# Optimization experiments

Hardware: AMD Instinct MI355X
Metric: run time of the kernel (lower is better)

The kernel has to match this reference:

```python
import jax, jax.numpy as jnp
import numpy as np

NUM_HEADS = 8
NUM_GROUPS = 32
EPS = 1e-5


def group_norm(x, gamma, beta):
    # x: [B, C, H, W]; normalize over (C//G, H, W) within each of G groups
    B, C, H, W = x.shape
    xg = x.reshape(B, NUM_GROUPS, C // NUM_GROUPS, H, W)
    mean = xg.mean(axis=(2, 3, 4), keepdims=True)
    var = xg.var(axis=(2, 3, 4), keepdims=True)
    xn = ((xg - mean) * jax.lax.rsqrt(var + EPS)).reshape(B, C, H, W)
    return xn * gamma[None, :, None, None] + beta[None, :, None, None]


def setup_inputs() -> dict:
    key = jax.random.key(0)
    ks = jax.random.split(key, 7)
    B, C, H, W = 16, 512, 32, 32
    x = jax.random.normal(ks[0], (B, C, H, W), dtype=jnp.float32)
    gamma = jnp.ones((C,), dtype=jnp.float32)
    beta = jnp.zeros((C,), dtype=jnp.float32)
    # 1x1 convs == per-pixel linear layers
    w_qkv = jax.random.normal(ks[1], (3 * C, C), dtype=jnp.float32) * (1.0 / np.sqrt(C))
    b_qkv = jax.random.normal(ks[2], (3 * C,), dtype=jnp.float32) * 0.02
    w_proj = jax.random.normal(ks[3], (C, C), dtype=jnp.float32) * (1.0 / np.sqrt(C))
    b_proj = jax.random.normal(ks[4], (C,), dtype=jnp.float32) * 0.02
    return {"x": x, "gamma": gamma, "beta": beta, "w_qkv": w_qkv,
            "b_qkv": b_qkv, "w_proj": w_proj, "b_proj": b_proj}


def reference(x, gamma, beta, w_qkv, b_qkv, w_proj, b_proj):
    B, C, H, W = x.shape
    nh = NUM_HEADS
    d = C // nh
    N = H * W
    h = group_norm(x, gamma, beta)
    # 1x1 conv: [B,C,H,W] x [3C,C] -> [B,3C,H,W]
    qkv = jnp.einsum('bchw,oc->bohw', h, w_qkv) + b_qkv[None, :, None, None]
    qkv = qkv.reshape(B, 3, nh, d, N)  # matches torch reshape(B,3,heads,d,HW)
    q, k, v = qkv[:, 0], qkv[:, 1], qkv[:, 2]
    scale = d ** (-0.5)
    attn = jnp.einsum('bhdn,bhdm->bhnm', q, k) * scale  # [B,h,N,N]
    attn = jax.nn.softmax(attn, axis=-1)
    out = jnp.einsum('bhnm,bhdm->bhdn', attn, v)  # [B,h,d,N]
    out = out.reshape(B, C, H, W)
    proj = jnp.einsum('bchw,oc->bohw', out, w_proj) + b_proj[None, :, None, None]
    return x + proj
```

## Files before the change

### kernel.cpp

```cpp
#include <hip/hip_runtime.h>
#include <cstddef>

#define B_  16
#define C_  512
#define N_  1024

typedef __attribute__((ext_vector_type(8))) __bf16 bf16x8;
typedef __attribute__((ext_vector_type(4))) float f32x4;
typedef __attribute__((ext_vector_type(4))) short s16x4;

__device__ __forceinline__ unsigned short f2bf(float x) {
  unsigned u = __float_as_uint(x);
  return (unsigned short)((u + 0x7fffu + ((u >> 16) & 1u)) >> 16);
}
__device__ __forceinline__ float bf2f(unsigned short h) {
  return __uint_as_float(((unsigned)h) << 16);
}

#define GLDS16(g, l)                                                            \
  __builtin_amdgcn_global_load_lds(                                             \
      (const __attribute__((address_space(1))) void*)(g),                       \
      (__attribute__((address_space(3))) void*)(l), 16, 0, 0)

__global__ __launch_bounds__(256) void wconv_kernel(
    const float* __restrict__ wq, const float* __restrict__ wp,
    unsigned short* __restrict__ oq, unsigned short* __restrict__ op) {
  int i = blockIdx.x * 256 + threadIdx.x;
  const float4* src; unsigned short* dst; int off;
  if (i < 196608) { src = (const float4*)wq; dst = oq; off = i; }
  else            { src = (const float4*)wp; dst = op; off = i - 196608; }
  float4 v = src[off];
  union { unsigned short s[4]; ushort4 u; } o;
  o.s[0] = f2bf(v.x); o.s[1] = f2bf(v.y);
  o.s[2] = f2bf(v.z); o.s[3] = f2bf(v.w);
  *(ushort4*)(dst + (size_t)off * 4) = o.u;
}

__global__ __launch_bounds__(256) void gn_kernel(
    const float* __restrict__ x, const float* __restrict__ gamma,
    const float* __restrict__ beta, unsigned short* __restrict__ hT) {
  int bg = blockIdx.x;
  int b = bg >> 5, g = bg & 31;
  size_t base = ((size_t)b * C_ + (size_t)g * 16) * N_;
  const float4* x4 = (const float4*)(x + base);
  int tid = threadIdx.x;

  float sum = 0.f, sq = 0.f;
  float4 vv[16];
#pragma unroll
  for (int i = 0; i < 16; i++) {
    float4 v = x4[tid + i * 256];
    vv[i] = v;
    sum += v.x + v.y + v.z + v.w;
    sq  += v.x * v.x + v.y * v.y + v.z * v.z + v.w * v.w;
  }
#pragma unroll
  for (int off = 32; off > 0; off >>= 1) {
    sum += __shfl_down(sum, off, 64);
    sq  += __shfl_down(sq, off, 64);
  }
  __shared__ float sm[4], sv[4];
  int lane = tid & 63, w = tid >> 6;
  if (lane == 0) { sm[w] = sum; sv[w] = sq; }
  __syncthreads();
  if (tid == 0) {
    float s = sm[0] + sm[1] + sm[2] + sm[3];
    float q = sv[0] + sv[1] + sv[2] + sv[3];
    float mean = s * (1.f / 16384.f);
    float var  = q * (1.f / 16384.f) - mean * mean;
    sm[0] = mean;
    sv[0] = rsqrtf(var + 1e-5f);
  }
  __syncthreads();
  float mean = sm[0], rstd = sv[0];

  union { unsigned short s[16]; uint4 u[2]; } row[4];
#pragma unroll
  for (int i = 0; i < 16; i++) {
    int c = g * 16 + i;
    float ga = gamma[c] * rstd;
    float be = beta[c] - mean * ga;
    float4 v = vv[i];
    row[0].s[i] = f2bf(v.x * ga + be);
    row[1].s[i] = f2bf(v.y * ga + be);
    row[2].s[i] = f2bf(v.z * ga + be);
    row[3].s[i] = f2bf(v.w * ga + be);
  }
#pragma unroll
  for (int j = 0; j < 4; j++) {
    uint4* dst = (uint4*)(hT + ((size_t)b * N_ + 4 * tid + j) * C_ + g * 16);
    dst[0] = row[j].u[0];
    dst[1] = row[j].u[1];
  }
}

template <int OUT_BF16>
__global__ __launch_bounds__(256) void gemm_mfma(
    const unsigned short* __restrict__ Wb, const float* __restrict__ bias,
    const unsigned short* __restrict__ InT, const float* __restrict__ resid,
    void* __restrict__ Out, int M) {
  __shared__ __align__(16) unsigned short As[128 * 32];
  __shared__ __align__(16) unsigned short Bs[128 * 32];

  const int b = blockIdx.z;
  const int n0 = blockIdx.x * 128, m0 = blockIdx.y * 128;
  const int tid = threadIdx.x;
  const int lane = tid & 63, wave = tid >> 6;
  const int col = lane & 15, quad = lane >> 4;
  const int wm = (wave >> 1) << 6, wn = (wave & 1) << 6;

  const unsigned short* Ag = Wb + (size_t)m0 * C_;
  const unsigned short* Bg = InT + ((size_t)b * N_ + n0) * C_;

  const int r0 = tid >> 2, c0 = (tid & 3) << 3;

  f32x4 acc[4][4];
#pragma unroll
  for (int i = 0; i < 4; i++)
#pragma unroll
    for (int j = 0; j < 4; j++) acc[i][j] = f32x4{0.f, 0.f, 0.f, 0.f};

  for (int k0 = 0; k0 < C_; k0 += 32) {
    __syncthreads();
    GLDS16(Ag + (size_t)r0 * C_ + k0 + c0,        &As[tid * 8]);
    GLDS16(Ag + (size_t)(r0 + 64) * C_ + k0 + c0, &As[(tid + 256) * 8]);
    GLDS16(Bg + (size_t)r0 * C_ + k0 + c0,        &Bs[tid * 8]);
    GLDS16(Bg + (size_t)(r0 + 64) * C_ + k0 + c0, &Bs[(tid + 256) * 8]);
    __syncthreads();

    bf16x8 af[4], bfr[4];
#pragma unroll
    for (int mt = 0; mt < 4; mt++)
      af[mt] = *(const bf16x8*)&As[(wm + mt * 16 + col) * 32 + quad * 8];
#pragma unroll
    for (int nt = 0; nt < 4; nt++)
      bfr[nt] = *(const bf16x8*)&Bs[(wn + nt * 16 + col) * 32 + quad * 8];
#pragma unroll
    for (int mt = 0; mt < 4; mt++)
#pragma unroll
      for (int nt = 0; nt < 4; nt++)
        acc[mt][nt] = __builtin_amdgcn_mfma_f32_16x16x32_bf16(
            af[mt], bfr[nt], acc[mt][nt], 0, 0, 0);
  }

#pragma unroll
  for (int mt = 0; mt < 4; mt++) {
    int mbase = m0 + wm + mt * 16 + quad * 4;
#pragma unroll
    for (int nt = 0; nt < 4; nt++) {
      int n = n0 + wn + nt * 16 + col;
#pragma unroll
      for (int r = 0; r < 4; r++) {
        int m = mbase + r;
        float v = acc[mt][nt][r] + bias[m];
        size_t off = ((size_t)b * M + m) * N_ + n;
        if constexpr (OUT_BF16) {
          ((unsigned short*)Out)[off] = f2bf(v);
        } else {
          ((float*)Out)[off] = v + resid[off];
        }
      }
    }
  }
}

__global__ __launch_bounds__(256) void attn_mfma(
    const unsigned short* __restrict__ qkv, unsigned short* __restrict__ aoT) {
  __shared__ __align__(16) unsigned short Kt[64 * 72];
  __shared__ __align__(16) unsigned short Vs[64 * 72];

  const int tid = threadIdx.x;
  const int wave = tid >> 6, lane = tid & 63;
  const int quad = lane >> 4, col = lane & 15;
  const int b = blockIdx.z, hh = blockIdx.y;
  const int qblk = blockIdx.x * 256 + wave * 64;

  const unsigned short* qp = qkv + ((size_t)b * 1536 + hh * 64) * N_;
  const unsigned short* kp = qp + (size_t)512 * N_;
  const unsigned short* vp = qp + (size_t)1024 * N_;

  bf16x8 qf[4][2];
#pragma unroll
  for (int nt = 0; nt < 4; nt++) {
    int qg = qblk + nt * 16 + col;
#pragma unroll
    for (int ks = 0; ks < 2; ks++) {
      union { unsigned short s[8]; bf16x8 v; } t;
#pragma unroll
      for (int j = 0; j < 8; j++) {
        int d = ks * 32 + quad * 8 + j;
        t.s[j] = f2bf(0.125f * bf2f(qp[(size_t)d * N_ + qg]));
      }
      qf[nt][ks] = t.v;
    }
  }

  float l_i[4];
  f32x4 O[4][4];
#pragma unroll
  for (int nt = 0; nt < 4; nt++) {
    l_i[nt] = 0.f;
#pragma unroll
    for (int mt = 0; mt < 4; mt++) O[mt][nt] = f32x4{0.f, 0.f, 0.f, 0.f};
  }

  const int sc = tid & 15, sd0 = tid >> 4;

  for (int kt = 0; kt < 16; kt++) {
    __syncthreads();
#pragma unroll
    for (int i = 0; i < 4; i++) {
      int d = sd0 + 16 * i;
      ushort4 kv = *(const ushort4*)(kp + (size_t)d * N_ + kt * 64 + sc * 4);
      ushort4 vv = *(const ushort4*)(vp + (size_t)d * N_ + kt * 64 + sc * 4);
      int sw = (sc >> 1) & 7;
      int dcol = (((d >> 3) ^ sw) << 3) | (d & 7);
      Kt[(4 * sc + 0) * 72 + dcol] = kv.x;
      Kt[(4 * sc + 1) * 72 + dcol] = kv.y;
      Kt[(4 * sc + 2) * 72 + dcol] = kv.z;
      Kt[(4 * sc + 3) * 72 + dcol] = kv.w;
      unsigned short* vrow = &Vs[d * 72 + 4 * sc];
      vrow[0] = vv.x; vrow[1] = vv.y;
      vrow[2] = vv.z; vrow[3] = vv.w;
    }
    __syncthreads();

    bf16x8 kf[4][2];
#pragma unroll
    for (int mt = 0; mt < 4; mt++) {
      int key = 16 * mt + col;
      int swr = (key >> 3) & 7;
#pragma unroll
      for (int ks = 0; ks < 2; ks++)
        kf[mt][ks] = *(const bf16x8*)&Kt[key * 72 + (((ks * 4 + quad) ^ swr) << 3)];
    }
    s16x4 vf[4][4];
#pragma unroll
    for (int mt = 0; mt < 4; mt++)
#pragma unroll
      for (int kc = 0; kc < 4; kc++)
        vf[mt][kc] = *(const s16x4*)&Vs[(16 * mt + col) * 72 + 16 * kc + quad * 4];

#pragma unroll
    for (int nt = 0; nt < 4; nt++) {
      f32x4 sf[4];
#pragma unroll
      for (int mt = 0; mt < 4; mt++) sf[mt] = f32x4{0.f, 0.f, 0.f, 0.f};
#pragma unroll
      for (int ks = 0; ks < 2; ks++)
#pragma unroll
        for (int mt = 0; mt < 4; mt++)
          sf[mt] = __builtin_amdgcn_mfma_f32_16x16x32_bf16(kf[mt][ks], qf[nt][ks], sf[mt], 0, 0, 0);

      s16x4 pb[4];
      float lsum = 0.f;
#pragma unroll
      for (int kc = 0; kc < 4; kc++) {
        float e0 = __expf(sf[kc][0]);
        float e1 = __expf(sf[kc][1]);
        float e2 = __expf(sf[kc][2]);
        float e3 = __expf(sf[kc][3]);
        lsum += (e0 + e1) + (e2 + e3);
        unsigned lo = __builtin_amdgcn_perm(__float_as_uint(e1), __float_as_uint(e0), 0x07060302u);
        unsigned hi = __builtin_amdgcn_perm(__float_as_uint(e3), __float_as_uint(e2), 0x07060302u);
        union { unsigned u[2]; s16x4 v; } t;
        t.u[0] = lo; t.u[1] = hi;
        pb[kc] = t.v;
      }
      l_i[nt] += lsum;

#pragma unroll
      for (int kc = 0; kc < 4; kc++)
#pragma unroll
        for (int mt = 0; mt < 4; mt++)
          O[mt][nt] = __builtin_amdgcn_mfma_f32_16x16x16bf16_1k(vf[mt][kc], pb[kc], O[mt][nt], 0, 0, 0);
    }
  }

#pragma unroll
  for (int nt = 0; nt < 4; nt++) {
    float ls = l_i[nt];
    ls += __shfl_xor(ls, 16, 64);
    ls += __shfl_xor(ls, 32, 64);
    float inv = 1.f / ls;
    int qg = qblk + nt * 16 + col;
    unsigned short* dst = aoT + ((size_t)b * N_ + qg) * C_ + hh * 64;
#pragma unroll
    for (int mt = 0; mt < 4; mt++) {
      union { unsigned short s[4]; ushort4 v; } o;
#pragma unroll
      for (int r = 0; r < 4; r++) o.s[r] = f2bf(O[mt][nt][r] * inv);
      *(ushort4*)(dst + mt * 16 + quad * 4) = o.v;
    }
  }
}

extern "C" void kernel_launch(void* const* d_in, const int* in_sizes, int n_in,
                              void* d_out, int out_size, void* d_ws, size_t ws_size,
                              hipStream_t stream) {
  (void)in_sizes; (void)n_in; (void)out_size; (void)ws_size;
  const float* x      = (const float*)d_in[0];
  const float* gamma  = (const float*)d_in[1];
  const float* beta   = (const float*)d_in[2];
  const float* w_qkv  = (const float*)d_in[3];
  const float* b_qkv  = (const float*)d_in[4];
  const float* w_proj = (const float*)d_in[5];
  const float* b_proj = (const float*)d_in[6];
  float* out = (float*)d_out;

  unsigned short* hT   = (unsigned short*)d_ws;
  unsigned short* qkvb = hT + (size_t)B_ * N_ * C_;
  unsigned short* aoT  = hT;
  unsigned short* wqb  = qkvb + (size_t)B_ * 1536 * N_;
  unsigned short* wpb  = wqb + (size_t)1536 * 512;

  wconv_kernel<<<dim3(1024), dim3(256), 0, stream>>>(w_qkv, w_proj, wqb, wpb);
  gn_kernel<<<dim3(B_ * 32), dim3(256), 0, stream>>>(x, gamma, beta, hT);
  gemm_mfma<1><<<dim3(8, 12, 16), dim3(256), 0, stream>>>(
      wqb, b_qkv, hT, (const float*)nullptr, (void*)qkvb, 1536);
  attn_mfma<<<dim3(4, 8, 16), dim3(256), 0, stream>>>(qkvb, aoT);
  gemm_mfma<0><<<dim3(8, 4, 16), dim3(256), 0, stream>>>(
      wpb, b_proj, aoT, x, (void*)out, 512);
}
```

Measured before the change: 225.9 us.

## Write Q/K transposed from QKV GEMM and double-buffer V via async LDS loads

The QKV GEMM epilogue now writes Q and K in token-major layout with vectorized stores. Q is pre-scaled by the softmax scale times log2(e), so attention can use exp2 and load Q and K fragments directly from global memory. V keeps its channel-major layout and is staged into a swizzled, double-buffered LDS tile with global_load_lds, which removes the per-tile LDS transpose and one barrier. The PV product moves to the 16x16x32 MFMA by pairing key tiles. K fragments now come from global memory every tile, which may add memory traffic or latency in exchange for less LDS work.

```diff
diff --git a/kernel.cpp b/kernel.cpp
--- a/kernel.cpp
+++ b/kernel.cpp
@@ -4,17 +4,14 @@
 #define B_  16
 #define C_  512
 #define N_  1024
+#define QSC 0.18033688011112042f
 
 typedef __attribute__((ext_vector_type(8))) __bf16 bf16x8;
 typedef __attribute__((ext_vector_type(4))) float f32x4;
-typedef __attribute__((ext_vector_type(4))) short s16x4;
 
 __device__ __forceinline__ unsigned short f2bf(float x) {
   unsigned u = __float_as_uint(x);
   return (unsigned short)((u + 0x7fffu + ((u >> 16) & 1u)) >> 16);
-}
-__device__ __forceinline__ float bf2f(unsigned short h) {
-  return __uint_as_float(((unsigned)h) << 16);
 }
 
 #define GLDS16(g, l)                                                            \
@@ -94,11 +91,11 @@
   }
 }
 
-template <int OUT_BF16>
+template <int MODE>
 __global__ __launch_bounds__(256) void gemm_mfma(
     const unsigned short* __restrict__ Wb, const float* __restrict__ bias,
     const unsigned short* __restrict__ InT, const float* __restrict__ resid,
-    void* __restrict__ Out, int M) {
+    void* __restrict__ Out, void* __restrict__ Out2, int M) {
   __shared__ __align__(16) unsigned short As[128 * 32];
   __shared__ __align__(16) unsigned short Bs[128 * 32];
 
@@ -143,31 +140,60 @@
             af[mt], bfr[nt], acc[mt][nt], 0, 0, 0);
   }
 
-#pragma unroll
-  for (int mt = 0; mt < 4; mt++) {
-    int mbase = m0 + wm + mt * 16 + quad * 4;
-#pragma unroll
-    for (int nt = 0; nt < 4; nt++) {
-      int n = n0 + wn + nt * 16 + col;
-#pragma unroll
-      for (int r = 0; r < 4; r++) {
-        int m = mbase + r;
-        float v = acc[mt][nt][r] + bias[m];
-        size_t off = ((size_t)b * M + m) * N_ + n;
-        if constexpr (OUT_BF16) {
-          ((unsigned short*)Out)[off] = f2bf(v);
-        } else {
-          ((float*)Out)[off] = v + resid[off];
+  if constexpr (MODE == 0) {
+#pragma unroll
+    for (int mt = 0; mt < 4; mt++) {
+      int mbase = m0 + wm + mt * 16 + quad * 4;
+#pragma unroll
+      for (int nt = 0; nt < 4; nt++) {
+        int n = n0 + wn + nt * 16 + col;
+#pragma unroll
+        for (int r = 0; r < 4; r++) {
+          int m = mbase + r;
+          size_t off = ((size_t)b * M + m) * N_ + n;
+          ((float*)Out)[off] = acc[mt][nt][r] + bias[m] + resid[off];
         }
       }
     }
+  } else {
+    if (blockIdx.y < 8) {
+      float qs = (blockIdx.y < 4) ? QSC : 1.0f;
+#pragma unroll
+      for (int mt = 0; mt < 4; mt++) {
+        int mbase = m0 + wm + mt * 16 + quad * 4;
+#pragma unroll
+        for (int nt = 0; nt < 4; nt++) {
+          int n = n0 + wn + nt * 16 + col;
+          union { unsigned short s[4]; ushort4 v; } o;
+#pragma unroll
+          for (int r = 0; r < 4; r++)
+            o.s[r] = f2bf((acc[mt][nt][r] + bias[mbase + r]) * qs);
+          *(ushort4*)((unsigned short*)Out + ((size_t)b * N_ + n) * 1024 + mbase) = o.v;
+        }
+      }
+    } else {
+#pragma unroll
+      for (int mt = 0; mt < 4; mt++) {
+        int mbase = m0 + wm + mt * 16 + quad * 4;
+#pragma unroll
+        for (int nt = 0; nt < 4; nt++) {
+          int n = n0 + wn + nt * 16 + col;
+#pragma unroll
+          for (int r = 0; r < 4; r++) {
+            int m = mbase + r;
+            ((unsigned short*)Out2)[((size_t)b * 512 + (m - 1024)) * N_ + n] =
+                f2bf(acc[mt][nt][r] + bias[m]);
+          }
+        }
+      }
+    }
   }
 }
 
 __global__ __launch_bounds__(256) void attn_mfma(
-    const unsigned short* __restrict__ qkv, unsigned short* __restrict__ aoT) {
-  __shared__ __align__(16) unsigned short Kt[64 * 72];
-  __shared__ __align__(16) unsigned short Vs[64 * 72];
+    const unsigned short* __restrict__ qkT, const unsigned short* __restrict__ Vb,
+    unsigned short* __restrict__ aoT) {
+  __shared__ __align__(16) unsigned short Vs[2][64 * 64];
 
   const int tid = threadIdx.x;
   const int wave = tid >> 6, lane = tid & 63;
@@ -175,25 +201,19 @@
   const int b = blockIdx.z, hh = blockIdx.y;
   const int qblk = blockIdx.x * 256 + wave * 64;
 
-  const unsigned short* qp = qkv + ((size_t)b * 1536 + hh * 64) * N_;
-  const unsigned short* kp = qp + (size_t)512 * N_;
-  const unsigned short* vp = qp + (size_t)1024 * N_;
+  const unsigned short* qkrow = qkT + (size_t)b * N_ * 1024;
+  const unsigned short* vp = Vb + ((size_t)b * 512 + hh * 64) * N_;
 
   bf16x8 qf[4][2];
 #pragma unroll
   for (int nt = 0; nt < 4; nt++) {
-    int qg = qblk + nt * 16 + col;
-#pragma unroll
-    for (int ks = 0; ks < 2; ks++) {
-      union { unsigned short s[8]; bf16x8 v; } t;
-#pragma unroll
-      for (int j = 0; j < 8; j++) {
-        int d = ks * 32 + quad * 8 + j;
-        t.s[j] = f2bf(0.125f * bf2f(qp[(size_t)d * N_ + qg]));
-      }
-      qf[nt][ks] = t.v;
-    }
-  }
+    const unsigned short* qr = qkrow + (size_t)(qblk + nt * 16 + col) * 1024 + hh * 64;
+#pragma unroll
+    for (int ks = 0; ks < 2; ks++)
+      qf[nt][ks] = *(const bf16x8*)(qr + ks * 32 + quad * 8);
+  }
+
+  const int krow_base = 8 * (col >> 2) + (col & 3);
 
   float l_i[4];
   f32x4 O[4][4];
@@ -204,76 +224,72 @@
     for (int mt = 0; mt < 4; mt++) O[mt][nt] = f32x4{0.f, 0.f, 0.f, 0.f};
   }
 
-  const int sc = tid & 15, sd0 = tid >> 4;
+  const int sd = tid >> 3, ss = tid & 7;
+  const int sc0 = (ss ^ (sd & 7)) * 8;
+  const int sc1 = (ss ^ ((sd + 32) & 7)) * 8;
+
+#define STAGE_V(p, kt)                                                          \
+  do {                                                                          \
+    GLDS16(vp + (size_t)sd * N_ + (kt) * 64 + sc0, &Vs[p][tid * 8]);            \
+    GLDS16(vp + (size_t)(sd + 32) * N_ + (kt) * 64 + sc1,                       \
+           &Vs[p][(tid + 256) * 8]);                                            \
+  } while (0)
+
+  STAGE_V(0, 0);
 
   for (int kt = 0; kt < 16; kt++) {
+    const int p = kt & 1;
     __syncthreads();
-#pragma unroll
-    for (int i = 0; i < 4; i++) {
-      int d = sd0 + 16 * i;
-      ushort4 kv = *(const ushort4*)(kp + (size_t)d * N_ + kt * 64 + sc * 4);
-      ushort4 vv = *(const ushort4*)(vp + (size_t)d * N_ + kt * 64 + sc * 4);
-      int sw = (sc >> 1) & 7;
-      int dcol = (((d >> 3) ^ sw) << 3) | (d & 7);
-      Kt[(4 * sc + 0) * 72 + dcol] = kv.x;
-      Kt[(4 * sc + 1) * 72 + dcol] = kv.y;
-      Kt[(4 * sc + 2) * 72 + dcol] = kv.z;
-      Kt[(4 * sc + 3) * 72 + dcol] = kv.w;
-      unsigned short* vrow = &Vs[d * 72 + 4 * sc];
-      vrow[0] = vv.x; vrow[1] = vv.y;
-      vrow[2] = vv.z; vrow[3] = vv.w;
-    }
-    __syncthreads();
+    if (kt < 15) STAGE_V(p ^ 1, kt + 1);
 
     bf16x8 kf[4][2];
 #pragma unroll
+    for (int u = 0; u < 4; u++) {
+      int krow = kt * 64 + 32 * (u >> 1) + 4 * (u & 1) + krow_base;
+      const unsigned short* kr = qkrow + (size_t)krow * 1024 + 512 + hh * 64;
+#pragma unroll
+      for (int ks = 0; ks < 2; ks++)
+        kf[u][ks] = *(const bf16x8*)(kr + ks * 32 + quad * 8);
+    }
+
+    bf16x8 vf[4][2];
+#pragma unroll
     for (int mt = 0; mt < 4; mt++) {
-      int key = 16 * mt + col;
-      int swr = (key >> 3) & 7;
-#pragma unroll
-      for (int ks = 0; ks < 2; ks++)
-        kf[mt][ks] = *(const bf16x8*)&Kt[key * 72 + (((ks * 4 + quad) ^ swr) << 3)];
-    }
-    s16x4 vf[4][4];
-#pragma unroll
-    for (int mt = 0; mt < 4; mt++)
-#pragma unroll
-      for (int kc = 0; kc < 4; kc++)
-        vf[mt][kc] = *(const s16x4*)&Vs[(16 * mt + col) * 72 + 16 * kc + quad * 4];
+      int d = 16 * mt + col;
+#pragma unroll
+      for (int s = 0; s < 2; s++)
+        vf[mt][s] = *(const bf16x8*)&Vs[p][d * 64 + (((4 * s + quad) ^ (d & 7)) << 3)];
+    }
 
 #pragma unroll
     for (int nt = 0; nt < 4; nt++) {
-      f32x4 sf[4];
-#pragma unroll
-      for (int mt = 0; mt < 4; mt++) sf[mt] = f32x4{0.f, 0.f, 0.f, 0.f};
-#pragma unroll
-      for (int ks = 0; ks < 2; ks++)
+#pragma unroll
+      for (int s = 0; s < 2; s++) {
+        f32x4 sfA = f32x4{0.f, 0.f, 0.f, 0.f};
+        f32x4 sfB = f32x4{0.f, 0.f, 0.f, 0.f};
+#pragma unroll
+        for (int ks = 0; ks < 2; ks++) {
+          sfA = __builtin_amdgcn_mfma_f32_16x16x32_bf16(kf[2 * s][ks], qf[nt][ks], sfA, 0, 0, 0);
+          sfB = __builtin_amdgcn_mfma_f32_16x16x32_bf16(kf[2 * s + 1][ks], qf[nt][ks], sfB, 0, 0, 0);
+        }
+        float eA0 = __builtin_amdgcn_exp2f(sfA[0]);
+        float eA1 = __builtin_amdgcn_exp2f(sfA[1]);
+        float eA2 = __builtin_amdgcn_exp2f(sfA[2]);
+        float eA3 = __builtin_amdgcn_exp2f(sfA[3]);
+        float eB0 = __builtin_amdgcn_exp2f(sfB[0]);
+        float eB1 = __builtin_amdgcn_exp2f(sfB[1]);
+        float eB2 = __builtin_amdgcn_exp2f(sfB[2]);
+        float eB3 = __builtin_amdgcn_exp2f(sfB[3]);
+        l_i[nt] += ((eA0 + eA1) + (eA2 + eA3)) + ((eB0 + eB1) + (eB2 + eB3));
+        union { unsigned u[4]; bf16x8 v; } pf;
+        pf.u[0] = __builtin_amdgcn_perm(__float_as_uint(eA1), __float_as_uint(eA0), 0x07060302u);
+        pf.u[1] = __builtin_amdgcn_perm(__float_as_uint(eA3), __float_as_uint(eA2), 0x07060302u);
+        pf.u[2] = __builtin_amdgcn_perm(__float_as_uint(eB1), __float_as_uint(eB0), 0x07060302u);
+        pf.u[3] = __builtin_amdgcn_perm(__float_as_uint(eB3), __float_as_uint(eB2), 0x07060302u);
 #pragma unroll
         for (int mt = 0; mt < 4; mt++)
-          sf[mt] = __builtin_amdgcn_mfma_f32_16x16x32_bf16(kf[mt][ks], qf[nt][ks], sf[mt], 0, 0, 0);
-
-      s16x4 pb[4];
-      float lsum = 0.f;
-#pragma unroll
-      for (int kc = 0; kc < 4; kc++) {
-        float e0 = __expf(sf[kc][0]);
-        float e1 = __expf(sf[kc][1]);
-        float e2 = __expf(sf[kc][2]);
-        float e3 = __expf(sf[kc][3]);
-        lsum += (e0 + e1) + (e2 + e3);
-        unsigned lo = __builtin_amdgcn_perm(__float_as_uint(e1), __float_as_uint(e0), 0x07060302u);
-        unsigned hi = __builtin_amdgcn_perm(__float_as_uint(e3), __float_as_uint(e2), 0x07060302u);
-        union { unsigned u[2]; s16x4 v; } t;
-        t.u[0] = lo; t.u[1] = hi;
-        pb[kc] = t.v;
+          O[mt][nt] = __builtin_amdgcn_mfma_f32_16x16x32_bf16(vf[mt][s], pf.v, O[mt][nt], 0, 0, 0);
       }
-      l_i[nt] += lsum;
-
-#pragma unroll
-      for (int kc = 0; kc < 4; kc++)
-#pragma unroll
-        for (int mt = 0; mt < 4; mt++)
-          O[mt][nt] = __builtin_amdgcn_mfma_f32_16x16x16bf16_1k(vf[mt][kc], pb[kc], O[mt][nt], 0, 0, 0);
     }
   }
 
@@ -293,6 +309,7 @@
       *(ushort4*)(dst + mt * 16 + quad * 4) = o.v;
     }
   }
+#undef STAGE_V
 }
 
 extern "C" void kernel_launch(void* const* d_in, const int* in_sizes, int n_in,
@@ -308,17 +325,18 @@
   const float* b_proj = (const float*)d_in[6];
   float* out = (float*)d_out;
 
-  unsigned short* hT   = (unsigned short*)d_ws;
-  unsigned short* qkvb = hT + (size_t)B_ * N_ * C_;
-  unsigned short* aoT  = hT;
-  unsigned short* wqb  = qkvb + (size_t)B_ * 1536 * N_;
-  unsigned short* wpb  = wqb + (size_t)1536 * 512;
+  unsigned short* hT  = (unsigned short*)d_ws;
+  unsigned short* qkT = hT + (size_t)B_ * N_ * C_;
+  unsigned short* Vb  = qkT + (size_t)B_ * N_ * 1024;
+  unsigned short* aoT = hT;
+  unsigned short* wqb = Vb + (size_t)B_ * C_ * N_;
+  unsigned short* wpb = wqb + (size_t)1536 * 512;
 
   wconv_kernel<<<dim3(1024), dim3(256), 0, stream>>>(w_qkv, w_proj, wqb, wpb);
   gn_kernel<<<dim3(B_ * 32), dim3(256), 0, stream>>>(x, gamma, beta, hT);
   gemm_mfma<1><<<dim3(8, 12, 16), dim3(256), 0, stream>>>(
-      wqb, b_qkv, hT, (const float*)nullptr, (void*)qkvb, 1536);
-  attn_mfma<<<dim3(4, 8, 16), dim3(256), 0, stream>>>(qkvb, aoT);
+      wqb, b_qkv, hT, (const float*)nullptr, (void*)qkT, (void*)Vb, 1536);
+  attn_mfma<<<dim3(4, 8, 16), dim3(256), 0, stream>>>(qkT, Vb, aoT);
   gemm_mfma<0><<<dim3(8, 4, 16), dim3(256), 0, stream>>>(
-      wpb, b_proj, aoT, x, (void*)out, 512);
-}
+      wpb, b_proj, aoT, x, (void*)out, (void*)nullptr, 512);
+}
```

Measured after the change: 240.0 us. 6.2% more time.
